# Kernel tuning notes

Hardware: AMD Instinct MI355X
Metric: run time of the kernel (lower is better)

The kernel has to match this reference:

```python
import jax, jax.numpy as jnp
import numpy as np

TARGET_SIZE = (240, 320)
SCALE = 8
POS_MARGIN = 1.0
NEG_MARGIN = 0.2
POS_LAMBDA = 0.05
EPS = 1e-12


def _l2n(x, axis):
    # F.normalize(p=2): x / max(||x||, eps)
    n = jnp.sqrt(jnp.sum(x * x, axis=axis, keepdims=True))
    return x / jnp.maximum(n, EPS)


def _rodrigues(rv):
    # axis-angle [N,3] -> rotation matrix [N,3,3]
    theta = jnp.linalg.norm(rv, axis=-1, keepdims=True)
    k = rv / jnp.maximum(theta, EPS)
    kx, ky, kz = k[..., 0], k[..., 1], k[..., 2]
    z = jnp.zeros_like(kx)
    Km = jnp.stack([z, -kz, ky, kz, z, -kx, -ky, kx, z], axis=-1).reshape(rv.shape[:-1] + (3, 3))
    th = theta[..., None]
    I = jnp.eye(3, dtype=rv.dtype)
    return I + jnp.sin(th) * Km + (1.0 - jnp.cos(th)) * (Km @ Km)


def _plane_homography(rv0, t0, rv1, t1, n, d, K, Kinv):
    # plane-induced homography: H = K (R_0->1 - t_0->1 n^T / d) K^{-1}
    R0 = _rodrigues(rv0)
    R1 = _rodrigues(rv1)
    R = R1 @ jnp.swapaxes(R0, -1, -2)
    t = t1[..., None] - R @ t0[..., None]            # [N,3,1]
    return K @ (R - (t @ n) / d[..., None]) @ Kinv   # n:[N,1,3], d:[N,1]


def _scale_homography(H, origin, target):
    # sizes are (H, W); homography acts on (x, y, 1): H' = S H S^{-1}
    s = target / origin                               # [N,2] = (sy, sx)
    svec = jnp.stack([s[:, 1], s[:, 0], jnp.ones_like(s[:, 0])], axis=-1)  # (sx, sy, 1)
    return H * (svec[:, :, None] / svec[:, None, :])


def _coord_cells(Hc, Wc):
    xx, yy = jnp.meshgrid(jnp.arange(Wc), jnp.arange(Hc), indexing='xy')
    return jnp.stack([xx, yy], axis=-1).astype(jnp.float32) * SCALE  # [Hc,Wc,2] (x,y)


def _forward(pred_features, rotation_vector, translation_vectors, camera_nts,
             camera_depths, camera_Ks, camera_Kinvs, origin_sizes, interval_list):
    T, B, C = rotation_vector.shape[:3]
    TC = T * C
    Cf, Hc, Wc = pred_features.shape[-3:]
    M = Hc * Wc

    # permute [T,B,C,...] -> [T,C,B,...] -> flatten to [T*C,B,...] (matches torch permute+reshape)
    rv = jnp.transpose(rotation_vector, (0, 2, 1, 3)).reshape(TC, B, 3)
    tv = jnp.transpose(translation_vectors, (0, 2, 1, 3)).reshape(TC, B, 3)
    nts = jnp.transpose(camera_nts, (0, 2, 1, 3, 4)).reshape(TC, B, 1, 3)
    dep = jnp.transpose(camera_depths, (0, 2, 1, 3)).reshape(TC, B, 1)
    Ks = jnp.transpose(camera_Ks, (0, 2, 1, 3, 4)).reshape(TC, B, 3, 3)
    Kin = jnp.transpose(camera_Kinvs, (0, 2, 1, 3, 4)).reshape(TC, B, 3, 3)
    osz = jnp.transpose(origin_sizes, (0, 2, 1, 3)).reshape(TC, B, 2)

    coords = _coord_cells(Hc, Wc)                     # [Hc,Wc,2]
    target = jnp.asarray(TARGET_SIZE, jnp.float32)
    thresh = SCALE - 0.5

    def step(acc, xs):
        f0, f1, Htt = xs                              # f0,f1: [B,Cf,Hc,Wc], Htt: [B,3,3]
        d0 = _l2n(f0, 1)
        d1 = _l2n(f1, 1)
        dot = jax.nn.relu(jnp.einsum('bchw,bcHW->bhwHW', d0, d1))  # [B,Hc,Wc,Hc,Wc]
        dot = _l2n(dot.reshape(B, Hc, Wc, M), 3).reshape(B, Hc, Wc, Hc, Wc)
        dot = _l2n(dot.reshape(B, M, Hc, Wc), 1).reshape(B, Hc, Wc, Hc, Wc)
        pos = jax.nn.relu(POS_MARGIN - dot)
        neg = jax.nn.relu(dot - NEG_MARGIN)
        # warp frame-0 cell centers into frame 1
        pts = jnp.concatenate([jnp.broadcast_to(coords, (B, Hc, Wc, 2)),
                               jnp.ones((B, Hc, Wc, 1), f0.dtype)], axis=-1)
        w = jnp.einsum('bij,bhwj->bhwi', Htt, pts)
        z = w[..., 2:3]
        z = jnp.where(jnp.abs(z) < 1e-8, 1e-8, z)
        warped = w[..., :2] / z                       # [B,Hc,Wc,2]
        dist = jnp.linalg.norm(coords[None, None, None] - warped[:, :, :, None, None, :], axis=-1)
        mask = (dist <= thresh).astype(dot.dtype)     # [B,Hc,Wc,Hc,Wc]
        l = POS_LAMBDA * mask * pos + (1.0 - mask) * neg
        return acc + jnp.mean(l), None

    total = jnp.float32(0.0)
    for interval in interval_list:
        iv = int(interval)
        N = TC - iv
        flat = lambda a: a[:N].reshape((N * B,) + a.shape[2:])
        H_all = _plane_homography(flat(rv), flat(tv),
                                  rv[iv:].reshape(N * B, 3), tv[iv:].reshape(N * B, 3),
                                  flat(nts), flat(dep), flat(Ks), flat(Kin))
        H_all = _scale_homography(H_all, flat(osz), jnp.broadcast_to(target, (N * B, 2)))
        loss_i, _ = jax.lax.scan(step, jnp.float32(0.0),
                                 (pred_features[:N], pred_features[iv:], H_all.reshape(N, B, 3, 3)))
        total = total + loss_i / N
    return total / len(interval_list)


def setup_inputs() -> dict:
    key = jax.random.key(0)
    ks = jax.random.split(key, 8)
    T, B, C, Cf = 5, 2, 4, 32
    Hc, Wc = TARGET_SIZE[0] // SCALE, TARGET_SIZE[1] // SCALE
    pred = jax.random.normal(ks[0], (T * C, B, Cf, Hc, Wc), jnp.float32)
    rv = 0.1 * jax.random.normal(ks[1], (T, B, C, 3), jnp.float32)
    tv = 0.1 * jax.random.normal(ks[2], (T, B, C, 3), jnp.float32)
    nts = jnp.array([0.0, 0.0, -1.0], jnp.float32) + 0.05 * jax.random.normal(ks[3], (T, B, C, 1, 3), jnp.float32)
    dep = 1.0 + jax.random.uniform(ks[4], (T, B, C, 1), jnp.float32)
    fx = 300.0 + 200.0 * jax.random.uniform(ks[5], (T, B, C), jnp.float32)
    fy = fx * (0.95 + 0.1 * jax.random.uniform(ks[6], (T, B, C), jnp.float32))
    K = jnp.zeros((T, B, C, 3, 3), jnp.float32)
    K = K.at[..., 0, 0].set(fx).at[..., 1, 1].set(fy)
    K = K.at[..., 0, 2].set(320.0).at[..., 1, 2].set(240.0).at[..., 2, 2].set(1.0)
    Kinv = jnp.linalg.inv(K)
    osz = jnp.tile(jnp.array([480.0, 640.0], jnp.float32), (T, B, C, 1))
    return {
        'pred_features': pred,
        'rotation_vector': rv,
        'translation_vectors': tv,
        'camera_nts': nts,
        'camera_depths': dep,
        'camera_Ks': K,
        'camera_Kinvs': Kinv,
        'origin_sizes': osz,
        'interval_list': (1, 4),
    }


def reference(pred_features, rotation_vector, translation_vectors, camera_nts,
              camera_depths, camera_Ks, camera_Kinvs, origin_sizes, interval_list):
    return _forward(pred_features, rotation_vector, translation_vectors, camera_nts,
                    camera_depths, camera_Ks, camera_Kinvs, origin_sizes, interval_list)
```

## Files before the change

### kernel.cpp

```cpp
#include <hip/hip_runtime.h>
#include <math.h>

#define TT   5
#define CAM  4
#define TC   20
#define BB   2
#define CF   32
#define HC   30
#define WC   40
#define MM   1200
#define NMAX 19
#define EPSF 1e-12f
#define JT   75
#define RG   38
#define RGB  10
#define JSP  3
#define JQ   25
#define CT   5
#define REDB 16

typedef __attribute__((ext_vector_type(8))) short short8v;
typedef __attribute__((ext_vector_type(4))) float float4v;

__device__ inline unsigned short f2bf(float x) {
  unsigned int u = __float_as_uint(x);
  unsigned int r = (u + 0x7FFFu + ((u >> 16) & 1u)) >> 16;
  return (unsigned short)r;
}
__device__ inline float bf2f(unsigned short h) {
  return __uint_as_float(((unsigned int)h) << 16);
}

__device__ inline void rodrigues_d(const double rv[3], double R[9]) {
  double th = sqrt(rv[0]*rv[0] + rv[1]*rv[1] + rv[2]*rv[2]);
  double thc = fmax(th, 1e-12);
  double kx = rv[0] / thc, ky = rv[1] / thc, kz = rv[2] / thc;
  double st = sin(th), ct = cos(th);
  double Km[9] = { 0.0, -kz,  ky,  kz, 0.0, -kx,  -ky, kx, 0.0 };
  double K2[9];
  for (int r = 0; r < 3; ++r)
    for (int c = 0; c < 3; ++c)
      K2[r*3+c] = Km[r*3+0]*Km[0*3+c] + Km[r*3+1]*Km[1*3+c] + Km[r*3+2]*Km[2*3+c];
  for (int r = 0; r < 3; ++r)
    for (int c = 0; c < 3; ++c)
      R[r*3+c] = (r == c ? 1.0 : 0.0) + st * Km[r*3+c] + (1.0 - ct) * K2[r*3+c];
}
__device__ inline void mm3(const double* A, const double* B, double* C) {
  for (int r = 0; r < 3; ++r)
    for (int c = 0; c < 3; ++c)
      C[r*3+c] = A[r*3+0]*B[0*3+c] + A[r*3+1]*B[1*3+c] + A[r*3+2]*B[2*3+c];
}

__device__ inline bool decode_slot(int slot, const int* ivl, int& n, int& b, int& iv) {
  int ivi = slot / (NMAX * BB);
  int rem = slot % (NMAX * BB);
  n = rem / BB; b = rem % BB;
  iv = ivl[ivi];
  return n < TC - iv;
}

__global__ void k_prep(const float* __restrict__ pred, short8v* __restrict__ dsp,
                       const float* __restrict__ rv_, const float* __restrict__ tv_,
                       const float* __restrict__ nts_, const float* __restrict__ dep_,
                       const float* __restrict__ Ks_, const float* __restrict__ Kin_,
                       const float* __restrict__ osz_, const int* __restrict__ ivl,
                       float2* __restrict__ warped) {
  int bx = blockIdx.x;
  int tid = threadIdx.x;
  if (bx < TC * BB * 5) {
    int tb = bx / 5;
    int pix = (bx % 5) * 240 + tid;
    if (tid >= 240 || pix >= MM) return;
    const float* src = pred + (size_t)tb * CF * MM;
    short8v*     dst = dsp  + (size_t)tb * 4 * MM;
    float v[CF]; float ss = 0.f;
#pragma unroll
    for (int c = 0; c < CF; ++c) { float x = src[c * MM + pix]; v[c] = x; ss = fmaf(x, x, ss); }
    float inv = 1.f / fmaxf(sqrtf(ss), EPSF);
#pragma unroll
    for (int s = 0; s < 4; ++s) {
      short8v oh;
#pragma unroll
      for (int e = 0; e < 8; ++e) oh[e] = (short)f2bf(v[s*8+e] * inv);
      dst[(size_t)s * MM + pix] = oh;
    }
    return;
  }
  int slot = bx - TC * BB * 5;
  int n, b, iv;
  if (!decode_slot(slot, ivl, n, b, iv)) return;
  int q0 = n, q1 = n + iv;
  int t0 = q0 / CAM, c0 = q0 % CAM;
  int t1 = q1 / CAM, c1 = q1 % CAM;
  size_t e0 = (size_t)(t0 * BB + b) * CAM + c0;
  size_t e1 = (size_t)(t1 * BB + b) * CAM + c1;

  double rv0[3], tv0[3], rv1[3], tv1[3], nv[3];
  for (int k = 0; k < 3; ++k) {
    rv0[k] = rv_[e0*3 + k]; tv0[k] = tv_[e0*3 + k];
    rv1[k] = rv_[e1*3 + k]; tv1[k] = tv_[e1*3 + k];
    nv[k]  = nts_[e0*3 + k];
  }
  double d = dep_[e0];
  double K9[9], Ki9[9];
  for (int k = 0; k < 9; ++k) { K9[k] = Ks_[e0*9 + k]; Ki9[k] = Kin_[e0*9 + k]; }

  double R0[9], R1[9], R[9];
  rodrigues_d(rv0, R0);
  rodrigues_d(rv1, R1);
  for (int r = 0; r < 3; ++r)
    for (int c = 0; c < 3; ++c)
      R[r*3+c] = R1[r*3+0]*R0[c*3+0] + R1[r*3+1]*R0[c*3+1] + R1[r*3+2]*R0[c*3+2];
  double tvec[3];
  for (int r = 0; r < 3; ++r)
    tvec[r] = tv1[r] - (R[r*3+0]*tv0[0] + R[r*3+1]*tv0[1] + R[r*3+2]*tv0[2]);
  double Mid[9];
  for (int r = 0; r < 3; ++r)
    for (int c = 0; c < 3; ++c)
      Mid[r*3+c] = R[r*3+c] - tvec[r] * nv[c] / d;
  double T1[9], Hm[9];
  mm3(K9, Mid, T1);
  mm3(T1, Ki9, Hm);

  double osz0 = osz_[e0*2 + 0], osz1 = osz_[e0*2 + 1];
  double s0 = 240.0 / osz0, s1 = 320.0 / osz1;
  double sv[3] = { s1, s0, 1.0 };
  double Hs[9];
  for (int r = 0; r < 3; ++r)
    for (int c = 0; c < 3; ++c)
      Hs[r*3+c] = Hm[r*3+c] * sv[r] / sv[c];

  float2* wout = warped + (size_t)slot * MM;
  for (int cell = tid; cell < MM; cell += blockDim.x) {
    double x = (double)((cell % WC) * 8);
    double y = (double)((cell / WC) * 8);
    double wx = Hs[0]*x + Hs[1]*y + Hs[2];
    double wy = Hs[3]*x + Hs[4]*y + Hs[5];
    double wz = Hs[6]*x + Hs[7]*y + Hs[8];
    float z = (float)wz;
    if (fabsf(z) < 1e-8f) z = 1e-8f;
    wout[cell] = make_float2((float)wx / z, (float)wy / z);
  }
}

__device__ inline float4v s_tile1(short8v ah, short8v bh) {
  float4v acc = {0.f, 0.f, 0.f, 0.f};
  return __builtin_amdgcn_mfma_f32_16x16x32_bf16(ah, bh, acc, 0, 0, 0);
}

__global__ void __launch_bounds__(256) k_rnorm_p(const short8v* __restrict__ dsp,
                                                 const int* __restrict__ ivl,
                                                 float* __restrict__ prn) {
  int slot = blockIdx.x, jh = blockIdx.z;
  int n, b, iv;
  if (!decode_slot(slot, ivl, n, b, iv)) return;
  int wid = threadIdx.x >> 6, lane = threadIdx.x & 63;
  int rg = blockIdx.y * 4 + wid;
  if (rg >= RG) return;
  int q = lane >> 4, li = lane & 15;
  int base = rg * 32;
  bool v1 = (base + 16) < MM;
  int r16a = base, r16b = v1 ? base + 16 : base;
  const short8v* D0 = dsp + (size_t)(n * BB + b) * 4 * MM;
  const short8v* B0 = dsp + (size_t)((n + iv) * BB + b) * 4 * MM + (size_t)q * MM + li;
  short8v ah0 = D0[(size_t)q * MM + r16a + li];
  short8v ah1 = D0[(size_t)q * MM + r16b + li];
  int jt0 = jh * JQ, jtN = jt0 + JQ;
  short8v bA = B0[jt0 * 16];
  short8v bB = B0[min(jt0 + 1, JT - 1) * 16];
  float4v racc0 = {0.f, 0.f, 0.f, 0.f};
  float4v racc1 = {0.f, 0.f, 0.f, 0.f};
#pragma unroll 5
  for (int jt = jt0; jt < jtN; ++jt) {
    short8v bC = B0[min(jt + 2, JT - 1) * 16];
    float4v acc0 = s_tile1(ah0, bA);
    float4v acc1 = s_tile1(ah1, bA);
#pragma unroll
    for (int r = 0; r < 4; ++r) {
      float t0 = fmaxf(acc0[r], 0.f); racc0[r] = fmaf(t0, t0, racc0[r]);
      float t1 = fmaxf(acc1[r], 0.f); racc1[r] = fmaf(t1, t1, racc1[r]);
    }
    bA = bB; bB = bC;
  }
#pragma unroll
  for (int m = 1; m <= 8; m <<= 1)
#pragma unroll
    for (int r = 0; r < 4; ++r) {
      racc0[r] += __shfl_xor(racc0[r], m);
      racc1[r] += __shfl_xor(racc1[r], m);
    }
  if (li == 0) {
    float* o = prn + ((size_t)slot * JSP + jh) * MM;
#pragma unroll
    for (int r = 0; r < 4; ++r) o[r16a + q * 4 + r] = racc0[r];
    if (v1) {
#pragma unroll
      for (int r = 0; r < 4; ++r) o[r16b + q * 4 + r] = racc1[r];
    }
  }
}

__global__ void __launch_bounds__(256) k_rnorm_fin(const float* __restrict__ prn,
                                                   const int* __restrict__ ivl,
                                                   float* __restrict__ irn) {
  int slot = blockIdx.x;
  int n, b, iv;
  if (!decode_slot(slot, ivl, n, b, iv)) return;
  int row = blockIdx.y * 256 + threadIdx.x;
  if (row >= MM) return;
  const float* p = prn + (size_t)slot * JSP * MM;
  float s = p[row] + p[MM + row] + p[2 * MM + row];
  irn[(size_t)slot * MM + row] = 1.f / fmaxf(sqrtf(s), EPSF);
}

__global__ void __launch_bounds__(256) k_cnorm_p(const short8v* __restrict__ dsp,
                                                 const int* __restrict__ ivl,
                                                 const float* __restrict__ irn,
                                                 float* __restrict__ pcn) {
  int slot = blockIdx.x, jh = blockIdx.z;
  int n, b, iv;
  if (!decode_slot(slot, ivl, n, b, iv)) return;
  int wid = threadIdx.x >> 6, lane = threadIdx.x & 63;
  int rg = blockIdx.y * 4 + wid;
  if (rg >= RG) return;
  int q = lane >> 4, li = lane & 15;
  int base = rg * 32;
  bool v1 = (base + 16) < MM;
  int c16a = base, c16b = v1 ? base + 16 : base;
  const short8v* D1 = dsp + (size_t)((n + iv) * BB + b) * 4 * MM;
  const short8v* B0 = dsp + (size_t)(n * BB + b) * 4 * MM + (size_t)q * MM + li;
  short8v ah0 = D1[(size_t)q * MM + c16a + li];
  short8v ah1 = D1[(size_t)q * MM + c16b + li];
  const float* irnS = irn + (size_t)slot * MM + li;
  int jt0 = jh * JQ, jtN = jt0 + JQ;
  short8v bA = B0[jt0 * 16];
  short8v bB = B0[min(jt0 + 1, JT - 1) * 16];
  float irA = irnS[jt0 * 16];
  float irB = irnS[min(jt0 + 1, JT - 1) * 16];
  float4v cacc0 = {0.f, 0.f, 0.f, 0.f};
  float4v cacc1 = {0.f, 0.f, 0.f, 0.f};
#pragma unroll 5
  for (int jt = jt0; jt < jtN; ++jt) {
    short8v bC = B0[min(jt + 2, JT - 1) * 16];
    float irC = irnS[min(jt + 2, JT - 1) * 16];
    float4v acc0 = s_tile1(ah0, bA);
    float4v acc1 = s_tile1(ah1, bA);
#pragma unroll
    for (int r = 0; r < 4; ++r) {
      float t0 = fmaxf(acc0[r], 0.f) * irA; cacc0[r] = fmaf(t0, t0, cacc0[r]);
      float t1 = fmaxf(acc1[r], 0.f) * irA; cacc1[r] = fmaf(t1, t1, cacc1[r]);
    }
    bA = bB; bB = bC; irA = irB; irB = irC;
  }
#pragma unroll
  for (int m = 1; m <= 8; m <<= 1)
#pragma unroll
    for (int r = 0; r < 4; ++r) {
      cacc0[r] += __shfl_xor(cacc0[r], m);
      cacc1[r] += __shfl_xor(cacc1[r], m);
    }
  if (li == 0) {
    float* o = pcn + ((size_t)slot * JSP + jh) * MM;
#pragma unroll
    for (int r = 0; r < 4; ++r) o[c16a + q * 4 + r] = cacc0[r];
    if (v1) {
#pragma unroll
      for (int r = 0; r < 4; ++r) o[c16b + q * 4 + r] = cacc1[r];
    }
  }
}

__global__ void __launch_bounds__(256) k_cnorm_fin(const float* __restrict__ pcn,
                                                   const int* __restrict__ ivl,
                                                   float* __restrict__ icn) {
  int slot = blockIdx.x;
  int n, b, iv;
  if (!decode_slot(slot, ivl, n, b, iv)) return;
  int col = blockIdx.y * 256 + threadIdx.x;
  if (col >= MM) return;
  const float* p = pcn + (size_t)slot * JSP * MM;
  float s = p[col] + p[MM + col] + p[2 * MM + col];
  icn[(size_t)slot * MM + col] = 1.f / fmaxf(sqrtf(s), EPSF);
}

__global__ void __launch_bounds__(256) k_loss(const short8v* __restrict__ dsp,
                                              const int* __restrict__ ivl,
                                              const float* __restrict__ irn,
                                              const float* __restrict__ icn,
                                              int niv,
                                              double* __restrict__ partials) {
  int slot = blockIdx.x, jh = blockIdx.z;
  int wid = threadIdx.x >> 6, lane = threadIdx.x & 63;
  int rg = blockIdx.y * 4 + wid;
  if (rg >= RG) return;
  size_t pidx = ((size_t)slot * RG + rg) * JSP + jh;
  int n, b, iv;
  if (!decode_slot(slot, ivl, n, b, iv)) {
    if (lane == 0) partials[pidx] = 0.0;
    return;
  }
  int q = lane >> 4, li = lane & 15;
  int base = rg * 32;
  bool v1 = (base + 16) < MM;
  int r16a = base, r16b = v1 ? base + 16 : base;
  const short8v* D0 = dsp + (size_t)(n * BB + b) * 4 * MM;
  const short8v* B0 = dsp + (size_t)((n + iv) * BB + b) * 4 * MM + (size_t)q * MM + li;
  short8v ah0 = D0[(size_t)q * MM + r16a + li];
  short8v ah1 = D0[(size_t)q * MM + r16b + li];
  float uA[4], uB[4];
#pragma unroll
  for (int r = 0; r < 4; ++r) {
    uA[r] = irn[(size_t)slot * MM + r16a + q * 4 + r];
    uB[r] = v1 ? irn[(size_t)slot * MM + r16b + q * 4 + r] : 0.f;
  }
  const float* icnS = icn + (size_t)slot * MM + li;
  int jt0 = jh * JQ, jtN = jt0 + JQ;
  short8v bA = B0[jt0 * 16];
  short8v bB = B0[min(jt0 + 1, JT - 1) * 16];
  float icA = icnS[jt0 * 16];
  float icB = icnS[min(jt0 + 1, JT - 1) * 16];
  float lacc0 = 0.f, lacc1 = 0.f;
#pragma unroll 5
  for (int jt = jt0; jt < jtN; ++jt) {
    short8v bC = B0[min(jt + 2, JT - 1) * 16];
    float icC = icnS[min(jt + 2, JT - 1) * 16];
    float4v acc0 = s_tile1(ah0, bA);
    float4v acc1 = s_tile1(ah1, bA);
#pragma unroll
    for (int r = 0; r < 4; ++r) {
      lacc0 += fmaxf(fmaf(acc0[r], icA * uA[r], -0.2f), 0.f);
      lacc1 += fmaxf(fmaf(acc1[r], icA * uB[r], -0.2f), 0.f);
    }
    bA = bB; bB = bC; icA = icB; icB = icC;
  }
  float lacc = lacc0 + lacc1;
#pragma unroll
  for (int off = 32; off > 0; off >>= 1) lacc += __shfl_xor(lacc, off);
  if (lane == 0) {
    double scale = 1.0 / ((double)(TC - iv) * BB * (double)MM * (double)MM * (double)niv);
    partials[pidx] = (double)lacc * scale;
  }
}

__global__ void __launch_bounds__(256) k_corr(const short8v* __restrict__ dsp,
                                              const int* __restrict__ ivl,
                                              const float* __restrict__ irn,
                                              const float* __restrict__ icn,
                                              const float2* __restrict__ warped,
                                              int niv,
                                              double* __restrict__ partials2) {
  __shared__ double swsum[4];
  int slot = blockIdx.x, tile = blockIdx.y;
  int t = threadIdx.x;
  int n, b, iv;
  bool valid = decode_slot(slot, ivl, n, b, iv);
  double corr = 0.0;
  int row = tile * 256 + t;
  if (valid && row < MM) {
    float2 wp = warped[(size_t)slot * MM + row];
    int kx0 = max(0, (int)ceilf((wp.x - 7.5f) * 0.125f));
    int kx1 = min(WC - 1, (int)floorf((wp.x + 7.5f) * 0.125f));
    int ky0 = max(0, (int)ceilf((wp.y - 7.5f) * 0.125f));
    int ky1 = min(HC - 1, (int)floorf((wp.y + 7.5f) * 0.125f));
    if (kx0 <= kx1 && ky0 <= ky1) {
      const short8v* D0 = dsp + (size_t)(n * BB + b) * 4 * MM;
      const short8v* D1 = dsp + (size_t)((n + iv) * BB + b) * 4 * MM;
      float a[CF];
#pragma unroll
      for (int qq = 0; qq < 4; ++qq) {
        short8v h = D0[(size_t)qq * MM + row];
#pragma unroll
        for (int e = 0; e < 8; ++e) a[qq * 8 + e] = bf2f((unsigned short)h[e]);
      }
      float ir = irn[(size_t)slot * MM + row];
      float fcorr = 0.f;
      for (int ky = ky0; ky <= ky1; ++ky) {
        for (int kx = kx0; kx <= kx1; ++kx) {
          float dx = (float)(kx * 8) - wp.x;
          float dy = (float)(ky * 8) - wp.y;
          if (fmaf(dx, dx, dy * dy) <= 56.25f) {
            int j = ky * WC + kx;
            float dot = 0.f;
#pragma unroll
            for (int qq = 0; qq < 4; ++qq) {
              short8v h1 = D1[(size_t)qq * MM + j];
#pragma unroll
              for (int e = 0; e < 8; ++e)
                dot = fmaf(a[qq * 8 + e], bf2f((unsigned short)h1[e]), dot);
            }
            float s = fmaxf(dot, 0.f);
            float D = s * ir * icn[(size_t)slot * MM + j];
            fcorr += 0.05f * fmaxf(1.f - D, 0.f) - fmaxf(D - 0.2f, 0.f);
          }
        }
      }
      double scale = 1.0 / ((double)(TC - iv) * BB * (double)MM * (double)MM * (double)niv);
      corr = (double)fcorr * scale;
    }
  }
#pragma unroll
  for (int off = 32; off > 0; off >>= 1) corr += __shfl_down(corr, off);
  int wid = t >> 6, lane = t & 63;
  if (lane == 0) swsum[wid] = corr;
  __syncthreads();
  if (t == 0) partials2[(size_t)slot * CT + tile] = swsum[0] + swsum[1] + swsum[2] + swsum[3];
}

__global__ void __launch_bounds__(256) k_red1(const double* __restrict__ p1, int n1,
                                              const double* __restrict__ p2, int n2,
                                              double* __restrict__ red) {
  __shared__ double sw[4];
  int t = threadIdx.x, blk = blockIdx.x;
  double s = 0.0;
  for (int i = blk * 256 + t; i < n1; i += REDB * 256) s += p1[i];
  for (int i = blk * 256 + t; i < n2; i += REDB * 256) s += p2[i];
#pragma unroll
  for (int off = 32; off > 0; off >>= 1) s += __shfl_down(s, off);
  int wid = t >> 6, lane = t & 63;
  if (lane == 0) sw[wid] = s;
  __syncthreads();
  if (t == 0) red[blk] = sw[0] + sw[1] + sw[2] + sw[3];
}

__global__ void k_red2(const double* __restrict__ red, float* __restrict__ out) {
  int lane = threadIdx.x;
  double s = (lane < REDB) ? red[lane] : 0.0;
#pragma unroll
  for (int off = 32; off > 0; off >>= 1) s += __shfl_down(s, off);
  if (lane == 0) out[0] = (float)s;
}

extern "C" void kernel_launch(void* const* d_in, const int* in_sizes, int n_in,
                              void* d_out, int out_size, void* d_ws, size_t ws_size,
                              hipStream_t stream) {
  const float* pred = (const float*)d_in[0];
  const float* rv   = (const float*)d_in[1];
  const float* tv   = (const float*)d_in[2];
  const float* nts  = (const float*)d_in[3];
  const float* dep  = (const float*)d_in[4];
  const float* Ks   = (const float*)d_in[5];
  const float* Kin  = (const float*)d_in[6];
  const float* osz  = (const float*)d_in[7];
  const int*   ivl  = (const int*)d_in[8];
  int niv = in_sizes[8];
  int slots = niv * NMAX * BB;

  char* ws = (char*)d_ws;
  size_t off = 0;
  short8v* dsp = (short8v*)(ws + off);  off += (size_t)TC * BB * 4 * MM * 16;
  float2* warped = (float2*)(ws + off); off += (size_t)slots * MM * 8;
  float* prn = (float*)(ws + off);      off += (size_t)slots * JSP * MM * 4;
  float* pcn = (float*)(ws + off);      off += (size_t)slots * JSP * MM * 4;
  float* irn = (float*)(ws + off);      off += (size_t)slots * MM * 4;
  float* icn = (float*)(ws + off);      off += (size_t)slots * MM * 4;
  off = (off + 255) & ~(size_t)255;
  double* partials = (double*)(ws + off);  off += (size_t)slots * RG * JSP * 8;
  double* partials2 = (double*)(ws + off); off += (size_t)slots * CT * 8;
  double* red = (double*)(ws + off);       off += (size_t)REDB * 8;

  int n1 = slots * RG * JSP;
  int n2 = slots * CT;

  hipLaunchKernelGGL(k_prep, dim3(TC * BB * 5 + slots), dim3(256), 0, stream,
                     pred, dsp, rv, tv, nts, dep, Ks, Kin, osz, ivl, warped);
  dim3 sgrid(slots, RGB, JSP);
  dim3 fgrid(slots, CT);
  hipLaunchKernelGGL(k_rnorm_p, sgrid, dim3(256), 0, stream, dsp, ivl, prn);
  hipLaunchKernelGGL(k_rnorm_fin, fgrid, dim3(256), 0, stream, prn, ivl, irn);
  hipLaunchKernelGGL(k_cnorm_p, sgrid, dim3(256), 0, stream, dsp, ivl, irn, pcn);
  hipLaunchKernelGGL(k_cnorm_fin, fgrid, dim3(256), 0, stream, pcn, ivl, icn);
  hipLaunchKernelGGL(k_loss, sgrid, dim3(256), 0, stream, dsp, ivl, irn, icn, niv, partials);
  hipLaunchKernelGGL(k_corr, fgrid, dim3(256), 0, stream,
                     dsp, ivl, irn, icn, warped, niv, partials2);
  hipLaunchKernelGGL(k_red1, dim3(REDB), dim3(256), 0, stream, partials, n1, partials2, n2, red);
  hipLaunchKernelGGL(k_red2, dim3(1), dim3(64), 0, stream, red, (float*)d_out);
}
```

Before: 80.93 us.

## Widen per-wave row tile to 64 rows and rebalance column split

Each wave now holds four 16-row A fragments instead of two, so every B fragment it loads feeds four MFMAs instead of two. The column range is split five ways rather than three to keep the grid size roughly the same, and the partial-buffer layouts and finalize kernels are updated to match. This halves B-fragment loads per MFMA and the number of row groups. In exchange each wave uses more registers, and the partial sums are spread over more column chunks.

```diff
diff --git a/kernel.cpp b/kernel.cpp
--- a/kernel.cpp
+++ b/kernel.cpp
@@ -12,10 +12,10 @@
 #define NMAX 19
 #define EPSF 1e-12f
 #define JT   75
-#define RG   38
-#define RGB  10
-#define JSP  3
-#define JQ   25
+#define RG4  19
+#define RGB4 5
+#define JSP  5
+#define JQ   15
 #define CT   5
 #define REDB 16
 
@@ -156,47 +156,54 @@
   if (!decode_slot(slot, ivl, n, b, iv)) return;
   int wid = threadIdx.x >> 6, lane = threadIdx.x & 63;
   int rg = blockIdx.y * 4 + wid;
-  if (rg >= RG) return;
+  if (rg >= RG4) return;
   int q = lane >> 4, li = lane & 15;
-  int base = rg * 32;
-  bool v1 = (base + 16) < MM;
-  int r16a = base, r16b = v1 ? base + 16 : base;
+  int base = rg * 64;
   const short8v* D0 = dsp + (size_t)(n * BB + b) * 4 * MM;
   const short8v* B0 = dsp + (size_t)((n + iv) * BB + b) * 4 * MM + (size_t)q * MM + li;
-  short8v ah0 = D0[(size_t)q * MM + r16a + li];
-  short8v ah1 = D0[(size_t)q * MM + r16b + li];
+  bool vt[4]; int rt[4];
+  short8v ah[4];
+  float4v racc[4];
+#pragma unroll
+  for (int t = 0; t < 4; ++t) {
+    int rb = base + t * 16;
+    vt[t] = rb < MM;
+    rt[t] = vt[t] ? rb : 0;
+    ah[t] = D0[(size_t)q * MM + rt[t] + li];
+    racc[t] = (float4v){0.f, 0.f, 0.f, 0.f};
+  }
   int jt0 = jh * JQ, jtN = jt0 + JQ;
   short8v bA = B0[jt0 * 16];
   short8v bB = B0[min(jt0 + 1, JT - 1) * 16];
-  float4v racc0 = {0.f, 0.f, 0.f, 0.f};
-  float4v racc1 = {0.f, 0.f, 0.f, 0.f};
-#pragma unroll 5
+#pragma unroll 3
   for (int jt = jt0; jt < jtN; ++jt) {
     short8v bC = B0[min(jt + 2, JT - 1) * 16];
-    float4v acc0 = s_tile1(ah0, bA);
-    float4v acc1 = s_tile1(ah1, bA);
-#pragma unroll
-    for (int r = 0; r < 4; ++r) {
-      float t0 = fmaxf(acc0[r], 0.f); racc0[r] = fmaf(t0, t0, racc0[r]);
-      float t1 = fmaxf(acc1[r], 0.f); racc1[r] = fmaf(t1, t1, racc1[r]);
+#pragma unroll
+    for (int t = 0; t < 4; ++t) {
+      float4v acc = s_tile1(ah[t], bA);
+#pragma unroll
+      for (int r = 0; r < 4; ++r) {
+        float x = fmaxf(acc[r], 0.f);
+        racc[t][r] = fmaf(x, x, racc[t][r]);
+      }
     }
     bA = bB; bB = bC;
   }
 #pragma unroll
   for (int m = 1; m <= 8; m <<= 1)
 #pragma unroll
-    for (int r = 0; r < 4; ++r) {
-      racc0[r] += __shfl_xor(racc0[r], m);
-      racc1[r] += __shfl_xor(racc1[r], m);
-    }
+    for (int t = 0; t < 4; ++t)
+#pragma unroll
+      for (int r = 0; r < 4; ++r)
+        racc[t][r] += __shfl_xor(racc[t][r], m);
   if (li == 0) {
     float* o = prn + ((size_t)slot * JSP + jh) * MM;
 #pragma unroll
-    for (int r = 0; r < 4; ++r) o[r16a + q * 4 + r] = racc0[r];
-    if (v1) {
-#pragma unroll
-      for (int r = 0; r < 4; ++r) o[r16b + q * 4 + r] = racc1[r];
-    }
+    for (int t = 0; t < 4; ++t)
+      if (vt[t]) {
+#pragma unroll
+        for (int r = 0; r < 4; ++r) o[rt[t] + q * 4 + r] = racc[t][r];
+      }
   }
 }
 
@@ -209,7 +216,9 @@
   int row = blockIdx.y * 256 + threadIdx.x;
   if (row >= MM) return;
   const float* p = prn + (size_t)slot * JSP * MM;
-  float s = p[row] + p[MM + row] + p[2 * MM + row];
+  float s = 0.f;
+#pragma unroll
+  for (int k = 0; k < JSP; ++k) s += p[k * MM + row];
   irn[(size_t)slot * MM + row] = 1.f / fmaxf(sqrtf(s), EPSF);
 }
 
@@ -222,51 +231,58 @@
   if (!decode_slot(slot, ivl, n, b, iv)) return;
   int wid = threadIdx.x >> 6, lane = threadIdx.x & 63;
   int rg = blockIdx.y * 4 + wid;
-  if (rg >= RG) return;
+  if (rg >= RG4) return;
   int q = lane >> 4, li = lane & 15;
-  int base = rg * 32;
-  bool v1 = (base + 16) < MM;
-  int c16a = base, c16b = v1 ? base + 16 : base;
+  int base = rg * 64;
   const short8v* D1 = dsp + (size_t)((n + iv) * BB + b) * 4 * MM;
   const short8v* B0 = dsp + (size_t)(n * BB + b) * 4 * MM + (size_t)q * MM + li;
-  short8v ah0 = D1[(size_t)q * MM + c16a + li];
-  short8v ah1 = D1[(size_t)q * MM + c16b + li];
+  bool vt[4]; int rt[4];
+  short8v ah[4];
+  float4v cacc[4];
+#pragma unroll
+  for (int t = 0; t < 4; ++t) {
+    int rb = base + t * 16;
+    vt[t] = rb < MM;
+    rt[t] = vt[t] ? rb : 0;
+    ah[t] = D1[(size_t)q * MM + rt[t] + li];
+    cacc[t] = (float4v){0.f, 0.f, 0.f, 0.f};
+  }
   const float* irnS = irn + (size_t)slot * MM + li;
   int jt0 = jh * JQ, jtN = jt0 + JQ;
   short8v bA = B0[jt0 * 16];
   short8v bB = B0[min(jt0 + 1, JT - 1) * 16];
   float irA = irnS[jt0 * 16];
   float irB = irnS[min(jt0 + 1, JT - 1) * 16];
-  float4v cacc0 = {0.f, 0.f, 0.f, 0.f};
-  float4v cacc1 = {0.f, 0.f, 0.f, 0.f};
-#pragma unroll 5
+#pragma unroll 3
   for (int jt = jt0; jt < jtN; ++jt) {
     short8v bC = B0[min(jt + 2, JT - 1) * 16];
     float irC = irnS[min(jt + 2, JT - 1) * 16];
-    float4v acc0 = s_tile1(ah0, bA);
-    float4v acc1 = s_tile1(ah1, bA);
-#pragma unroll
-    for (int r = 0; r < 4; ++r) {
-      float t0 = fmaxf(acc0[r], 0.f) * irA; cacc0[r] = fmaf(t0, t0, cacc0[r]);
-      float t1 = fmaxf(acc1[r], 0.f) * irA; cacc1[r] = fmaf(t1, t1, cacc1[r]);
+#pragma unroll
+    for (int t = 0; t < 4; ++t) {
+      float4v acc = s_tile1(ah[t], bA);
+#pragma unroll
+      for (int r = 0; r < 4; ++r) {
+        float x = fmaxf(acc[r], 0.f) * irA;
+        cacc[t][r] = fmaf(x, x, cacc[t][r]);
+      }
     }
     bA = bB; bB = bC; irA = irB; irB = irC;
   }
 #pragma unroll
   for (int m = 1; m <= 8; m <<= 1)
 #pragma unroll
-    for (int r = 0; r < 4; ++r) {
-      cacc0[r] += __shfl_xor(cacc0[r], m);
-      cacc1[r] += __shfl_xor(cacc1[r], m);
-    }
+    for (int t = 0; t < 4; ++t)
+#pragma unroll
+      for (int r = 0; r < 4; ++r)
+        cacc[t][r] += __shfl_xor(cacc[t][r], m);
   if (li == 0) {
     float* o = pcn + ((size_t)slot * JSP + jh) * MM;
 #pragma unroll
-    for (int r = 0; r < 4; ++r) o[c16a + q * 4 + r] = cacc0[r];
-    if (v1) {
-#pragma unroll
-      for (int r = 0; r < 4; ++r) o[c16b + q * 4 + r] = cacc1[r];
-    }
+    for (int t = 0; t < 4; ++t)
+      if (vt[t]) {
+#pragma unroll
+        for (int r = 0; r < 4; ++r) o[rt[t] + q * 4 + r] = cacc[t][r];
+      }
   }
 }
 
@@ -279,7 +295,9 @@
   int col = blockIdx.y * 256 + threadIdx.x;
   if (col >= MM) return;
   const float* p = pcn + (size_t)slot * JSP * MM;
-  float s = p[col] + p[MM + col] + p[2 * MM + col];
+  float s = 0.f;
+#pragma unroll
+  for (int k = 0; k < JSP; ++k) s += p[k * MM + col];
   icn[(size_t)slot * MM + col] = 1.f / fmaxf(sqrtf(s), EPSF);
 }
 
@@ -292,26 +310,28 @@
   int slot = blockIdx.x, jh = blockIdx.z;
   int wid = threadIdx.x >> 6, lane = threadIdx.x & 63;
   int rg = blockIdx.y * 4 + wid;
-  if (rg >= RG) return;
-  size_t pidx = ((size_t)slot * RG + rg) * JSP + jh;
+  if (rg >= RG4) return;
+  size_t pidx = ((size_t)slot * RG4 + rg) * JSP + jh;
   int n, b, iv;
   if (!decode_slot(slot, ivl, n, b, iv)) {
     if (lane == 0) partials[pidx] = 0.0;
     return;
   }
   int q = lane >> 4, li = lane & 15;
-  int base = rg * 32;
-  bool v1 = (base + 16) < MM;
-  int r16a = base, r16b = v1 ? base + 16 : base;
+  int base = rg * 64;
   const short8v* D0 = dsp + (size_t)(n * BB + b) * 4 * MM;
   const short8v* B0 = dsp + (size_t)((n + iv) * BB + b) * 4 * MM + (size_t)q * MM + li;
-  short8v ah0 = D0[(size_t)q * MM + r16a + li];
-  short8v ah1 = D0[(size_t)q * MM + r16b + li];
-  float uA[4], uB[4];
-#pragma unroll
-  for (int r = 0; r < 4; ++r) {
-    uA[r] = irn[(size_t)slot * MM + r16a + q * 4 + r];
-    uB[r] = v1 ? irn[(size_t)slot * MM + r16b + q * 4 + r] : 0.f;
+  short8v ah[4];
+  float u[4][4];
+#pragma unroll
+  for (int t = 0; t < 4; ++t) {
+    int rb = base + t * 16;
+    bool vt = rb < MM;
+    int rtc = vt ? rb : 0;
+    ah[t] = D0[(size_t)q * MM + rtc + li];
+#pragma unroll
+    for (int r = 0; r < 4; ++r)
+      u[t][r] = vt ? irn[(size_t)slot * MM + rtc + q * 4 + r] : 0.f;
   }
   const float* icnS = icn + (size_t)slot * MM + li;
   int jt0 = jh * JQ, jtN = jt0 + JQ;
@@ -320,16 +340,18 @@
   float icA = icnS[jt0 * 16];
   float icB = icnS[min(jt0 + 1, JT - 1) * 16];
   float lacc0 = 0.f, lacc1 = 0.f;
-#pragma unroll 5
+#pragma unroll 3
   for (int jt = jt0; jt < jtN; ++jt) {
     short8v bC = B0[min(jt + 2, JT - 1) * 16];
     float icC = icnS[min(jt + 2, JT - 1) * 16];
-    float4v acc0 = s_tile1(ah0, bA);
-    float4v acc1 = s_tile1(ah1, bA);
-#pragma unroll
-    for (int r = 0; r < 4; ++r) {
-      lacc0 += fmaxf(fmaf(acc0[r], icA * uA[r], -0.2f), 0.f);
-      lacc1 += fmaxf(fmaf(acc1[r], icA * uB[r], -0.2f), 0.f);
+#pragma unroll
+    for (int t = 0; t < 4; ++t) {
+      float4v acc = s_tile1(ah[t], bA);
+      float s0 = fmaxf(fmaf(acc[0], icA * u[t][0], -0.2f), 0.f)
+               + fmaxf(fmaf(acc[1], icA * u[t][1], -0.2f), 0.f);
+      float s1 = fmaxf(fmaf(acc[2], icA * u[t][2], -0.2f), 0.f)
+               + fmaxf(fmaf(acc[3], icA * u[t][3], -0.2f), 0.f);
+      lacc0 += s0; lacc1 += s1;
     }
     bA = bB; bB = bC; icA = icB; icB = icC;
   }
@@ -454,16 +476,16 @@
   float* irn = (float*)(ws + off);      off += (size_t)slots * MM * 4;
   float* icn = (float*)(ws + off);      off += (size_t)slots * MM * 4;
   off = (off + 255) & ~(size_t)255;
-  double* partials = (double*)(ws + off);  off += (size_t)slots * RG * JSP * 8;
+  double* partials = (double*)(ws + off);  off += (size_t)slots * RG4 * JSP * 8;
   double* partials2 = (double*)(ws + off); off += (size_t)slots * CT * 8;
   double* red = (double*)(ws + off);       off += (size_t)REDB * 8;
 
-  int n1 = slots * RG * JSP;
+  int n1 = slots * RG4 * JSP;
   int n2 = slots * CT;
 
   hipLaunchKernelGGL(k_prep, dim3(TC * BB * 5 + slots), dim3(256), 0, stream,
                      pred, dsp, rv, tv, nts, dep, Ks, Kin, osz, ivl, warped);
-  dim3 sgrid(slots, RGB, JSP);
+  dim3 sgrid(slots, RGB4, JSP);
   dim3 fgrid(slots, CT);
   hipLaunchKernelGGL(k_rnorm_p, sgrid, dim3(256), 0, stream, dsp, ivl, prn);
   hipLaunchKernelGGL(k_rnorm_fin, fgrid, dim3(256), 0, stream, prn, ivl, irn);
```

After: 76.90 us. 1.05x faster.
